# Optimization experiments

Measured on AMD Instinct MI355X. Metric: run time of the kernel, lower is better.

Reference implementation:

```python
import jax, jax.numpy as jnp
import numpy as np

POOL_SIZES = (1, 3, 6, 8)
EPS = 1e-5


def conv1x1(x, W, b):
    # x: [b, cin, h, w], W: [cout, cin], b: [cout]
    return jnp.einsum('bchw,oc->bohw', x, W) + b[None, :, None, None]


def ppm(x):
    # x: [b, c, h, w] -> [b, c, S] with S = sum(p*p); H,W divisible by each p
    b, c, h, w = x.shape
    outs = []
    for p in POOL_SIZES:
        pooled = x.reshape(b, c, p, h // p, p, w // p).mean(axis=(3, 5))
        outs.append(pooled.reshape(b, c, p * p))
    return jnp.concatenate(outs, axis=-1)


def setup_inputs() -> dict:
    key = jax.random.key(0)
    ks = jax.random.split(key, 8)
    B, Cin, H, W = 4, 512, 120, 120
    Ck, Cv, Cout = 256, 256, 512
    x = jax.random.normal(ks[0], (B, Cin, H, W), dtype=jnp.float32)
    sc = lambda cin: 1.0 / np.sqrt(cin)
    Wk = jax.random.normal(ks[1], (Ck, Cin), dtype=jnp.float32) * sc(Cin)
    bk = jnp.zeros((Ck,), jnp.float32)
    gamma = jnp.ones((Ck,), jnp.float32)
    beta = jnp.zeros((Ck,), jnp.float32)
    mean = jax.random.normal(ks[2], (Ck,), dtype=jnp.float32) * 0.1
    var = jax.random.uniform(ks[3], (Ck,), dtype=jnp.float32, minval=0.5, maxval=1.5)
    Wv = jax.random.normal(ks[4], (Cv, Cin), dtype=jnp.float32) * sc(Cin)
    bv = jnp.zeros((Cv,), jnp.float32)
    # original inits Conv_Out to zero; use random weights for a nontrivial baseline
    Wo = jax.random.normal(ks[5], (Cout, Cv), dtype=jnp.float32) * sc(Cv)
    bo = jnp.zeros((Cout,), jnp.float32)
    return {'x': x, 'Wk': Wk, 'bk': bk, 'gamma': gamma, 'beta': beta,
            'mean': mean, 'var': var, 'Wv': Wv, 'bv': bv, 'Wo': Wo, 'bo': bo}


def reference(x, Wk, bk, gamma, beta, mean, var, Wv, bv, Wo, bo):
    b, _, h, w = x.shape
    ck = Wk.shape[0]
    cv = Wv.shape[0]
    # shared Conv_Key / Conv_Query: conv1x1 -> BN (inference) -> ReLU
    kq = conv1x1(x, Wk, bk)
    inv = gamma / jnp.sqrt(var + EPS)
    kq = jax.nn.relu(kq * inv[None, :, None, None] + (beta - mean * inv)[None, :, None, None])
    value = ppm(conv1x1(x, Wv, bv)).transpose(0, 2, 1)      # [b, S, cv]
    key = ppm(kq)                                            # [b, ck, S]
    query = kq.reshape(b, ck, h * w).transpose(0, 2, 1)      # [b, hw, ck]
    scores = jnp.einsum('bnc,bcs->bns', query, key) * (ck ** -0.5)
    attn = jax.nn.softmax(scores, axis=-1)                   # [b, hw, S]
    agg = jnp.einsum('bns,bsv->bnv', attn, value)            # [b, hw, cv]
    agg = agg.transpose(0, 2, 1).reshape(b, cv, h, w)
    return conv1x1(agg, Wo, bo)
```

## Files before the change

### kernel.cpp

```cpp
#include <hip/hip_runtime.h>
#include <cstdint>
#include <cstddef>

#define HW 14400
#define WIDTH 120
#define S_TOT 110

typedef unsigned short u16;
typedef __attribute__((ext_vector_type(8))) short bf16x8;
typedef __attribute__((ext_vector_type(4))) float f32x4;

__device__ __forceinline__ u16 f2bf(float x) {
  unsigned u = __float_as_uint(x);
  unsigned r = (u + 0x7fffu + ((u >> 16) & 1u)) >> 16;
  return (u16)r;
}
__device__ __forceinline__ float bf2f(u16 h) {
  return __uint_as_float((unsigned)h << 16);
}

__device__ __forceinline__ void async16(void* lds, const void* g) {
  __builtin_amdgcn_global_load_lds(
      (const __attribute__((address_space(1))) void*)g,
      (__attribute__((address_space(3))) void*)lds, 16, 0, 0);
}

__global__ __launch_bounds__(256) void pool_kernel(const float* __restrict__ in,
                                                   float* __restrict__ outp) {
  __shared__ float part[576];
  const float* plane = in + (size_t)blockIdx.x * HW;
  int t = threadIdx.x;
  for (int bb = t; bb < 576; bb += 256) {
    int by = bb / 24, bx = bb % 24;
    const float* p0 = plane + (by * 5) * WIDTH + bx * 5;
    float s = 0.f;
#pragma unroll
    for (int yy = 0; yy < 5; ++yy)
#pragma unroll
      for (int xx = 0; xx < 5; ++xx) s += p0[yy * WIDTH + xx];
    part[bb] = s;
  }
  __syncthreads();
  if (t < S_TOT) {
    float s = 0.f;
    if (t == 0) {
      for (int i = 0; i < 576; ++i) s += part[i];
      s *= (1.f / 14400.f);
    } else if (t < 10) {
      int idx = t - 1, i = idx / 3, j = idx % 3;
      for (int a = 0; a < 8; ++a)
        for (int c = 0; c < 8; ++c) s += part[(i * 8 + a) * 24 + (j * 8 + c)];
      s *= (1.f / 1600.f);
    } else if (t < 46) {
      int idx = t - 10, i = idx / 6, j = idx % 6;
      for (int a = 0; a < 4; ++a)
        for (int c = 0; c < 4; ++c) s += part[(i * 4 + a) * 24 + (j * 4 + c)];
      s *= (1.f / 400.f);
    } else {
      int idx = t - 46, i = idx / 8, j = idx % 8;
      for (int a = 0; a < 3; ++a)
        for (int c = 0; c < 3; ++c) s += part[(i * 3 + a) * 24 + (j * 3 + c)];
      s *= (1.f / 225.f);
    }
    outp[(size_t)blockIdx.x * S_TOT + t] = s;
  }
}

__global__ __launch_bounds__(256) void convert_w(const float* __restrict__ in,
                                                 u16* __restrict__ hi,
                                                 u16* __restrict__ lo, int n) {
  int i = blockIdx.x * 256 + threadIdx.x;
  if (i < n) {
    float v = in[i];
    u16 h = f2bf(v);
    hi[i] = h;
    lo[i] = f2bf(v - bf2f(h));
  }
}

template <int CIN>
__global__ __launch_bounds__(256) void convert_t(const float* __restrict__ X,
                                                 u16* __restrict__ xth,
                                                 u16* __restrict__ xtl) {
  __shared__ float ls[64][65];
  int b = blockIdx.z;
  int n0 = blockIdx.x * 64, k0 = blockIdx.y * 64;
  int t = threadIdx.x;
  int rt = t >> 4, c4 = (t & 15) * 4;
#pragma unroll
  for (int rr = 0; rr < 4; ++rr) {
    int kk = rr * 16 + rt;
    float4 v = *(const float4*)&X[((size_t)(b * CIN + k0 + kk)) * HW + n0 + c4];
    ls[kk][c4] = v.x; ls[kk][c4 + 1] = v.y; ls[kk][c4 + 2] = v.z; ls[kk][c4 + 3] = v.w;
  }
  __syncthreads();
#pragma unroll
  for (int rr = 0; rr < 4; ++rr) {
    int nn = rr * 16 + rt;
    float v0 = ls[c4 + 0][nn], v1 = ls[c4 + 1][nn], v2 = ls[c4 + 2][nn], v3 = ls[c4 + 3][nn];
    ushort4 oh, ol;
    oh.x = f2bf(v0); ol.x = f2bf(v0 - bf2f(oh.x));
    oh.y = f2bf(v1); ol.y = f2bf(v1 - bf2f(oh.y));
    oh.z = f2bf(v2); ol.z = f2bf(v2 - bf2f(oh.z));
    oh.w = f2bf(v3); ol.w = f2bf(v3 - bf2f(oh.w));
    size_t idx = ((size_t)(b * HW + n0 + nn)) * CIN + k0 + c4;
    *(ushort4*)&xth[idx] = oh;
    *(ushort4*)&xtl[idx] = ol;
  }
}

template <int K, int M_TOT, bool BNRELU>
__global__ __launch_bounds__(512, 4) void gemm_mfma(
    const u16* __restrict__ Ah, const u16* __restrict__ Al,
    const u16* __restrict__ Bh, const u16* __restrict__ Bl,
    float* __restrict__ C,
    const float* __restrict__ p0, const float* __restrict__ p1,
    const float* __restrict__ p2, const float* __restrict__ p3,
    const float* __restrict__ p4) {
  constexpr int NSTEP = K / 32;
  __shared__ alignas(16) u16 sA[2][16][512];
  __shared__ alignas(16) u16 sB[2][24][512];

  int t = threadIdx.x, w = t >> 6, l = t & 63;
  int wm = w >> 2, wn = w & 3;
  int b = blockIdx.z;
  int n0 = blockIdx.x * 192;
  int m0 = blockIdx.y * 128;

  int fr = l & 15, fkc = l >> 4;
  const size_t bOff = (size_t)b * HW;

  auto stage = [&](int ks, int buf) {
    int k0 = ks * 32;
#pragma unroll
    for (int c = 0; c < 5; ++c) {
      int i = w * 5 + c;
      const u16* g;
      u16* d;
      if (i < 8) {
        g = Ah + (size_t)(m0 + i * 16 + fr) * K + k0 + fkc * 8;
        d = &sA[buf][i][0];
      } else if (i < 16) {
        g = Al + (size_t)(m0 + (i - 8) * 16 + fr) * K + k0 + fkc * 8;
        d = &sA[buf][i][0];
      } else if (i < 28) {
        g = Bh + (bOff + n0 + (i - 16) * 16 + fr) * (size_t)K + k0 + fkc * 8;
        d = &sB[buf][i - 16][0];
      } else {
        g = Bl + (bOff + n0 + (i - 28) * 16 + fr) * (size_t)K + k0 + fkc * 8;
        d = &sB[buf][i - 16][0];
      }
      async16(d, g);
    }
  };

  f32x4 acc[4][3];
#pragma unroll
  for (int i = 0; i < 4; ++i)
#pragma unroll
    for (int j = 0; j < 3; ++j) acc[i][j] = (f32x4){0.f, 0.f, 0.f, 0.f};

  stage(0, 0);

  for (int ks = 0; ks < NSTEP; ++ks) {
    __syncthreads();
    if (ks + 1 < NSTEP) stage(ks + 1, (ks + 1) & 1);
    int cur = ks & 1;
    bf16x8 bh[3], bl[3];
#pragma unroll
    for (int nt = 0; nt < 3; ++nt) {
      bh[nt] = *(const bf16x8*)&sB[cur][wn * 3 + nt][l * 8];
      bl[nt] = *(const bf16x8*)&sB[cur][12 + wn * 3 + nt][l * 8];
    }
#pragma unroll
    for (int mt = 0; mt < 4; ++mt) {
      bf16x8 ah = *(const bf16x8*)&sA[cur][wm * 4 + mt][l * 8];
      bf16x8 al = *(const bf16x8*)&sA[cur][8 + wm * 4 + mt][l * 8];
#pragma unroll
      for (int nt = 0; nt < 3; ++nt) {
        acc[mt][nt] = __builtin_amdgcn_mfma_f32_16x16x32_bf16(ah, bh[nt], acc[mt][nt], 0, 0, 0);
        acc[mt][nt] = __builtin_amdgcn_mfma_f32_16x16x32_bf16(ah, bl[nt], acc[mt][nt], 0, 0, 0);
        acc[mt][nt] = __builtin_amdgcn_mfma_f32_16x16x32_bf16(al, bh[nt], acc[mt][nt], 0, 0, 0);
      }
    }
  }

#pragma unroll
  for (int mt = 0; mt < 4; ++mt) {
    int mb = m0 + (wm * 4 + mt) * 16 + (l >> 4) * 4;
    float iv[4], ad[4];
    if (BNRELU) {
      float4 g0 = *(const float4*)&p0[mb];
      float4 g1 = *(const float4*)&p1[mb];
      float4 g2 = *(const float4*)&p2[mb];
      float4 g3 = *(const float4*)&p3[mb];
      float4 g4 = *(const float4*)&p4[mb];
      iv[0] = g1.x * rsqrtf(g4.x + 1e-5f);
      iv[1] = g1.y * rsqrtf(g4.y + 1e-5f);
      iv[2] = g1.z * rsqrtf(g4.z + 1e-5f);
      iv[3] = g1.w * rsqrtf(g4.w + 1e-5f);
      ad[0] = (g0.x - g3.x) * iv[0] + g2.x;
      ad[1] = (g0.y - g3.y) * iv[1] + g2.y;
      ad[2] = (g0.z - g3.z) * iv[2] + g2.z;
      ad[3] = (g0.w - g3.w) * iv[3] + g2.w;
    } else {
      float4 g0 = *(const float4*)&p0[mb];
      ad[0] = g0.x; ad[1] = g0.y; ad[2] = g0.z; ad[3] = g0.w;
    }
#pragma unroll
    for (int nt = 0; nt < 3; ++nt) {
      int n = n0 + (wn * 3 + nt) * 16 + fr;
#pragma unroll
      for (int r = 0; r < 4; ++r) {
        float v = acc[mt][nt][r];
        if (BNRELU)
          v = fmaxf(v * iv[r] + ad[r], 0.f);
        else
          v = v + ad[r];
        C[((size_t)(b * M_TOT) + mb + r) * HW + n] = v;
      }
    }
  }
}

__global__ __launch_bounds__(256) void value_kernel(
    const float* __restrict__ Wv, const float* __restrict__ xp,
    const float* __restrict__ bv, u16* __restrict__ vth,
    u16* __restrict__ vtl) {
  int b = blockIdx.x >> 7, s = blockIdx.x & 127;
  int t = threadIdx.x;
  size_t o = ((size_t)(b * 256 + t)) * 128 + s;
  if (s >= S_TOT) { vth[o] = 0; vtl[o] = 0; return; }
  __shared__ float xs[512];
  for (int i = t; i < 512; i += 256) xs[i] = xp[((size_t)b * 512 + i) * S_TOT + s];
  __syncthreads();
  float accv = 0.f;
  const float* wv = Wv + (size_t)t * 512;
  for (int k = 0; k < 512; k += 4) {
    float4 w4 = *(const float4*)&wv[k];
    accv += w4.x * xs[k] + w4.y * xs[k + 1] + w4.z * xs[k + 2] + w4.w * xs[k + 3];
  }
  accv += bv[t];
  u16 h = f2bf(accv);
  vth[o] = h;
  vtl[o] = f2bf(accv - bf2f(h));
}

__global__ __launch_bounds__(256) void convert_key(const float* __restrict__ keyp,
                                                   u16* __restrict__ kth,
                                                   u16* __restrict__ ktl) {
  int b = blockIdx.x;
  int t = threadIdx.x;
  for (int i = t; i < 128 * 256; i += 256) {
    int s = i >> 8, c = i & 255;
    float v = (s < S_TOT) ? keyp[((size_t)(b * 256 + c)) * S_TOT + s] : 0.f;
    u16 h = f2bf(v);
    size_t o = ((size_t)(b * 128 + s)) * 256 + c;
    kth[o] = h;
    ktl[o] = f2bf(v - bf2f(h));
  }
}

__global__ __launch_bounds__(256) void attn_mfma(
    const u16* __restrict__ qh, const u16* __restrict__ ql,
    const u16* __restrict__ kh, const u16* __restrict__ kl,
    const u16* __restrict__ vh, const u16* __restrict__ vl,
    u16* __restrict__ aggh, u16* __restrict__ aggl) {
  __shared__ alignas(16) u16 lds[17408];
  int b = blockIdx.y, pix0 = blockIdx.x * 64;
  int t = threadIdx.x, w = t >> 6, l = t & 63;
  int fr = l & 15, q = l >> 4;

  const u16* kbase_h = kh + (size_t)b * 128 * 256;
  const u16* kbase_l = kl + (size_t)b * 128 * 256;

  f32x4 acc[8];
#pragma unroll
  for (int st = 0; st < 8; ++st) acc[st] = (f32x4){0.f, 0.f, 0.f, 0.f};

  const u16* qbh = qh + ((size_t)(b * HW + pix0 + w * 16 + fr)) * 256 + q * 8;
  const u16* qbl = ql + ((size_t)(b * HW + pix0 + w * 16 + fr)) * 256 + q * 8;

  auto stageK = [&](int ks, int buf) {
    int c0 = ks * 32;
#pragma unroll
    for (int j = 0; j < 4; ++j) {
      int i = t + j * 256;
      int half = i >> 9;
      int idx = i & 511;
      int st = idx >> 6, ll = idx & 63;
      const u16* src = (half ? kbase_l : kbase_h) +
                       (st * 16 + (ll & 15)) * 256 + c0 + (ll >> 4) * 8;
      async16(&lds[buf * 8192 + half * 4096 + idx * 8], src);
    }
  };

  stageK(0, 0);
  for (int ks = 0; ks < 8; ++ks) {
    __syncthreads();
    if (ks < 7) stageK(ks + 1, (ks + 1) & 1);
    bf16x8 ah = *(const bf16x8*)(qbh + ks * 32);
    bf16x8 al = *(const bf16x8*)(qbl + ks * 32);
    const u16* kb = &lds[(ks & 1) * 8192 + l * 8];
#pragma unroll
    for (int st = 0; st < 8; ++st) {
      bf16x8 bh = *(const bf16x8*)(kb + st * 512);
      bf16x8 bl = *(const bf16x8*)(kb + 4096 + st * 512);
      acc[st] = __builtin_amdgcn_mfma_f32_16x16x32_bf16(ah, bh, acc[st], 0, 0, 0);
      acc[st] = __builtin_amdgcn_mfma_f32_16x16x32_bf16(ah, bl, acc[st], 0, 0, 0);
      acc[st] = __builtin_amdgcn_mfma_f32_16x16x32_bf16(al, bh, acc[st], 0, 0, 0);
    }
  }

#pragma unroll
  for (int st = 0; st < 8; ++st)
#pragma unroll
    for (int r = 0; r < 4; ++r) acc[st][r] *= 0.0625f;
  if (fr >= 14) {
#pragma unroll
    for (int r = 0; r < 4; ++r) acc[6][r] = -1e30f;
  }
#pragma unroll
  for (int r = 0; r < 4; ++r) acc[7][r] = -1e30f;

#pragma unroll
  for (int r = 0; r < 4; ++r) {
    float m = -1e30f;
#pragma unroll
    for (int st = 0; st < 8; ++st) m = fmaxf(m, acc[st][r]);
    m = fmaxf(m, __shfl_xor(m, 1));
    m = fmaxf(m, __shfl_xor(m, 2));
    m = fmaxf(m, __shfl_xor(m, 4));
    m = fmaxf(m, __shfl_xor(m, 8));
    float s = 0.f;
#pragma unroll
    for (int st = 0; st < 8; ++st) {
      float e = __expf(acc[st][r] - m);
      acc[st][r] = e;
      s += e;
    }
    s += __shfl_xor(s, 1);
    s += __shfl_xor(s, 2);
    s += __shfl_xor(s, 4);
    s += __shfl_xor(s, 8);
    float inv = 1.f / s;
#pragma unroll
    for (int st = 0; st < 8; ++st) acc[st][r] *= inv;
  }

  __syncthreads();

  int prow = w * 16 + q * 4;
#pragma unroll
  for (int st = 0; st < 8; ++st) {
    int s = st * 16 + fr;
#pragma unroll
    for (int r = 0; r < 4; ++r) {
      float v = acc[st][r];
      u16 h = f2bf(v);
      lds[(prow + r) * 136 + s] = h;
      lds[8704 + (prow + r) * 136 + s] = f2bf(v - bf2f(h));
    }
  }
  __syncthreads();

  f32x4 oacc[4][4];
#pragma unroll
  for (int nt = 0; nt < 4; ++nt)
#pragma unroll
    for (int pt = 0; pt < 4; ++pt) oacc[nt][pt] = (f32x4){0.f, 0.f, 0.f, 0.f};

  const u16* vbh = vh + ((size_t)(b * 256 + w * 64 + fr)) * 128 + q * 8;
  const u16* vbl = vl + ((size_t)(b * 256 + w * 64 + fr)) * 128 + q * 8;

#pragma unroll
  for (int kc = 0; kc < 4; ++kc) {
    bf16x8 ph[4], pl[4];
#pragma unroll
    for (int pt = 0; pt < 4; ++pt) {
      ph[pt] = *(const bf16x8*)&lds[(pt * 16 + fr) * 136 + kc * 32 + q * 8];
      pl[pt] = *(const bf16x8*)&lds[8704 + (pt * 16 + fr) * 136 + kc * 32 + q * 8];
    }
#pragma unroll
    for (int nt = 0; nt < 4; ++nt) {
      bf16x8 a_h = *(const bf16x8*)(vbh + (size_t)nt * 16 * 128 + kc * 32);
      bf16x8 a_l = *(const bf16x8*)(vbl + (size_t)nt * 16 * 128 + kc * 32);
#pragma unroll
      for (int pt = 0; pt < 4; ++pt) {
        oacc[nt][pt] = __builtin_amdgcn_mfma_f32_16x16x32_bf16(a_h, ph[pt], oacc[nt][pt], 0, 0, 0);
        oacc[nt][pt] = __builtin_amdgcn_mfma_f32_16x16x32_bf16(a_h, pl[pt], oacc[nt][pt], 0, 0, 0);
        oacc[nt][pt] = __builtin_amdgcn_mfma_f32_16x16x32_bf16(a_l, ph[pt], oacc[nt][pt], 0, 0, 0);
      }
    }
  }

#pragma unroll
  for (int nt = 0; nt < 4; ++nt) {
#pragma unroll
    for (int pt = 0; pt < 4; ++pt) {
      ushort4 oh, ol;
      float v0 = oacc[nt][pt][0], v1 = oacc[nt][pt][1];
      float v2 = oacc[nt][pt][2], v3 = oacc[nt][pt][3];
      oh.x = f2bf(v0); ol.x = f2bf(v0 - bf2f(oh.x));
      oh.y = f2bf(v1); ol.y = f2bf(v1 - bf2f(oh.y));
      oh.z = f2bf(v2); ol.z = f2bf(v2 - bf2f(oh.z));
      oh.w = f2bf(v3); ol.w = f2bf(v3 - bf2f(oh.w));
      size_t o = ((size_t)(b * HW + pix0 + pt * 16 + fr)) * 256 + (w * 4 + nt) * 16 + q * 4;
      *(ushort4*)&aggh[o] = oh;
      *(ushort4*)&aggl[o] = ol;
    }
  }
}

extern "C" void kernel_launch(void* const* d_in, const int* in_sizes, int n_in,
                              void* d_out, int out_size, void* d_ws, size_t ws_size,
                              hipStream_t stream) {
  (void)in_sizes; (void)n_in; (void)out_size; (void)ws_size;
  const float* x     = (const float*)d_in[0];
  const float* Wk    = (const float*)d_in[1];
  const float* bk    = (const float*)d_in[2];
  const float* gamma = (const float*)d_in[3];
  const float* beta  = (const float*)d_in[4];
  const float* mean  = (const float*)d_in[5];
  const float* var   = (const float*)d_in[6];
  const float* Wv    = (const float*)d_in[7];
  const float* bv    = (const float*)d_in[8];
  const float* Wo    = (const float*)d_in[9];
  const float* bo    = (const float*)d_in[10];
  float* out = (float*)d_out;

  char* p = (char*)d_ws;
  float* kq = (float*)p;      p += (size_t)14745600 * 4;
  u16* xth = (u16*)p;         p += (size_t)29491200 * 2;
  u16* xtl = (u16*)p;         p += (size_t)29491200 * 2;
  u16* wkh = (u16*)p;         p += 131072 * 2;
  u16* wkl = (u16*)p;         p += 131072 * 2;
  u16* woh = (u16*)p;         p += 131072 * 2;
  u16* wol = (u16*)p;         p += 131072 * 2;
  float* xp = (float*)p;      p += (size_t)4 * 512 * 110 * 4;
  float* keyp = (float*)p;    p += (size_t)4 * 256 * 110 * 4;
  u16* vth = (u16*)p;         p += (size_t)4 * 256 * 128 * 2;
  u16* vtl = (u16*)p;         p += (size_t)4 * 256 * 128 * 2;
  u16* kth = (u16*)p;         p += (size_t)4 * 128 * 256 * 2;
  u16* ktl = (u16*)p;         p += (size_t)4 * 128 * 256 * 2;
  u16* aggh = xth;
  u16* kqth = xth + (size_t)14745600;
  u16* aggl = xtl;
  u16* kqtl = xtl + (size_t)14745600;

  convert_w<<<512, 256, 0, stream>>>(Wk, wkh, wkl, 256 * 512);
  convert_w<<<512, 256, 0, stream>>>(Wo, woh, wol, 512 * 256);
  convert_t<512><<<dim3(225, 8, 4), 256, 0, stream>>>(x, xth, xtl);
  pool_kernel<<<dim3(4 * 512), dim3(256), 0, stream>>>(x, xp);
  value_kernel<<<dim3(4 * 128), dim3(256), 0, stream>>>(Wv, xp, bv, vth, vtl);
  gemm_mfma<512, 256, true><<<dim3(75, 2, 4), 512, 0, stream>>>(
      wkh, wkl, xth, xtl, kq, bk, gamma, beta, mean, var);
  convert_t<256><<<dim3(225, 4, 4), 256, 0, stream>>>(kq, kqth, kqtl);
  pool_kernel<<<dim3(4 * 256), dim3(256), 0, stream>>>(kq, keyp);
  convert_key<<<dim3(4), dim3(256), 0, stream>>>(keyp, kth, ktl);
  attn_mfma<<<dim3(225, 4), 256, 0, stream>>>(kqth, kqtl, kth, ktl, vth, vtl,
                                              aggh, aggl);
  gemm_mfma<256, 512, false><<<dim3(75, 4, 4), 512, 0, stream>>>(
      woh, wol, aggh, aggl, out, bo, nullptr, nullptr, nullptr, nullptr);
}
```

Before: 590.2 us.

## Triple-buffer GEMM LDS staging with vmcnt waits and MFMA priority boost

Moves the split-bf16 MFMA GEMM from double to triple buffering in LDS, prefetching two k-steps ahead. The full __syncthreads is replaced by an explicit s_waitcnt vmcnt(5) plus a raw barrier, so one stage of async loads can stay in flight. All A fragments are loaded before the MFMA burst, which runs at raised wave priority. LDS per block grows by half and launch bounds drop to 2 blocks per SM, which may reduce occupancy. Correctness also relies on the vmcnt count matching the five async loads issued per stage.

```diff
diff --git a/kernel.cpp b/kernel.cpp
--- a/kernel.cpp
+++ b/kernel.cpp
@@ -110,7 +110,7 @@
 }
 
 template <int K, int M_TOT, bool BNRELU>
-__global__ __launch_bounds__(512, 4) void gemm_mfma(
+__global__ __launch_bounds__(512, 2) void gemm_mfma(
     const u16* __restrict__ Ah, const u16* __restrict__ Al,
     const u16* __restrict__ Bh, const u16* __restrict__ Bl,
     float* __restrict__ C,
@@ -118,8 +118,8 @@
     const float* __restrict__ p2, const float* __restrict__ p3,
     const float* __restrict__ p4) {
   constexpr int NSTEP = K / 32;
-  __shared__ alignas(16) u16 sA[2][16][512];
-  __shared__ alignas(16) u16 sB[2][24][512];
+  __shared__ alignas(16) u16 sA[3][16][512];
+  __shared__ alignas(16) u16 sB[3][24][512];
 
   int t = threadIdx.x, w = t >> 6, l = t & 63;
   int wm = w >> 2, wn = w & 3;
@@ -130,7 +130,7 @@
   int fr = l & 15, fkc = l >> 4;
   const size_t bOff = (size_t)b * HW;
 
-  auto stage = [&](int ks, int buf) {
+  auto stage = [&](int ks, int slot) {
     int k0 = ks * 32;
 #pragma unroll
     for (int c = 0; c < 5; ++c) {
@@ -139,16 +139,16 @@
       u16* d;
       if (i < 8) {
         g = Ah + (size_t)(m0 + i * 16 + fr) * K + k0 + fkc * 8;
-        d = &sA[buf][i][0];
+        d = &sA[slot][i][0];
       } else if (i < 16) {
         g = Al + (size_t)(m0 + (i - 8) * 16 + fr) * K + k0 + fkc * 8;
-        d = &sA[buf][i][0];
+        d = &sA[slot][i][0];
       } else if (i < 28) {
         g = Bh + (bOff + n0 + (i - 16) * 16 + fr) * (size_t)K + k0 + fkc * 8;
-        d = &sB[buf][i - 16][0];
+        d = &sB[slot][i - 16][0];
       } else {
         g = Bl + (bOff + n0 + (i - 28) * 16 + fr) * (size_t)K + k0 + fkc * 8;
-        d = &sB[buf][i - 16][0];
+        d = &sB[slot][i - 16][0];
       }
       async16(d, g);
     }
@@ -161,28 +161,41 @@
     for (int j = 0; j < 3; ++j) acc[i][j] = (f32x4){0.f, 0.f, 0.f, 0.f};
 
   stage(0, 0);
+  stage(1, 1);
 
   for (int ks = 0; ks < NSTEP; ++ks) {
-    __syncthreads();
-    if (ks + 1 < NSTEP) stage(ks + 1, (ks + 1) & 1);
-    int cur = ks & 1;
+    if (ks + 1 < NSTEP)
+      asm volatile("s_waitcnt vmcnt(5)" ::: "memory");
+    else
+      asm volatile("s_waitcnt vmcnt(0)" ::: "memory");
+    __builtin_amdgcn_s_barrier();
+    __builtin_amdgcn_sched_barrier(0);
+
+    if (ks + 2 < NSTEP) stage(ks + 2, (ks + 2) % 3);
+
+    int cur = ks % 3;
     bf16x8 bh[3], bl[3];
 #pragma unroll
     for (int nt = 0; nt < 3; ++nt) {
       bh[nt] = *(const bf16x8*)&sB[cur][wn * 3 + nt][l * 8];
       bl[nt] = *(const bf16x8*)&sB[cur][12 + wn * 3 + nt][l * 8];
     }
+    bf16x8 ah[4], al[4];
 #pragma unroll
     for (int mt = 0; mt < 4; ++mt) {
-      bf16x8 ah = *(const bf16x8*)&sA[cur][wm * 4 + mt][l * 8];
-      bf16x8 al = *(const bf16x8*)&sA[cur][8 + wm * 4 + mt][l * 8];
+      ah[mt] = *(const bf16x8*)&sA[cur][wm * 4 + mt][l * 8];
+      al[mt] = *(const bf16x8*)&sA[cur][8 + wm * 4 + mt][l * 8];
+    }
+    __builtin_amdgcn_s_setprio(1);
+#pragma unroll
+    for (int mt = 0; mt < 4; ++mt)
 #pragma unroll
       for (int nt = 0; nt < 3; ++nt) {
-        acc[mt][nt] = __builtin_amdgcn_mfma_f32_16x16x32_bf16(ah, bh[nt], acc[mt][nt], 0, 0, 0);
-        acc[mt][nt] = __builtin_amdgcn_mfma_f32_16x16x32_bf16(ah, bl[nt], acc[mt][nt], 0, 0, 0);
-        acc[mt][nt] = __builtin_amdgcn_mfma_f32_16x16x32_bf16(al, bh[nt], acc[mt][nt], 0, 0, 0);
+        acc[mt][nt] = __builtin_amdgcn_mfma_f32_16x16x32_bf16(ah[mt], bh[nt], acc[mt][nt], 0, 0, 0);
+        acc[mt][nt] = __builtin_amdgcn_mfma_f32_16x16x32_bf16(ah[mt], bl[nt], acc[mt][nt], 0, 0, 0);
+        acc[mt][nt] = __builtin_amdgcn_mfma_f32_16x16x32_bf16(al[mt], bh[nt], acc[mt][nt], 0, 0, 0);
       }
-    }
+    __builtin_amdgcn_s_setprio(0);
   }
 
 #pragma unroll
```

Measured after the change: 560.0 us. 5.1% less time.
